# Kernel optimization log

Hardware: AMD Instinct MI355X
Metric: run time of the kernel (lower is better)

## Reference

```python
import jax, jax.numpy as jnp
import numpy as np
from jax import lax

T, B, IN, ND, H, L, C = 128, 64, 48, 3, 2048, 4, 10
MAG = 2.0
U_BOUND = float(np.power(10.0, np.log10(MAG) / T))
INI_IN2HID = 0.02
BN_EPS = 1e-5


def _indrnn_scan(xs, u):
    # xs: [T, B, H], u: [H]; h_t = relu(x_t + u * h_{t-1}), h_0 = 0
    def step(h, xt):
        h = jax.nn.relu(xt + u * h)
        return h, h
    _, hs = lax.scan(step, jnp.zeros_like(xs[0]), xs)
    return hs


def setup_inputs() -> dict:
    key = jax.random.key(0)
    ks = jax.random.split(key, 8)
    x = jax.random.normal(ks[0], (T, B, IN, ND), dtype=jnp.float32)
    W0 = jax.random.uniform(ks[1], (H, IN * ND), minval=-INI_IN2HID, maxval=INI_IN2HID, dtype=jnp.float32)
    Ws = jax.random.uniform(ks[2], (L - 1, H, H), minval=-INI_IN2HID, maxval=INI_IN2HID, dtype=jnp.float32)
    bs = jnp.zeros((L, H), dtype=jnp.float32)
    us = jax.random.uniform(ks[3], (L, H), minval=0.0, maxval=U_BOUND, dtype=jnp.float32)
    gammas = jnp.ones((L, H), dtype=jnp.float32)
    betas = jnp.zeros((L, H), dtype=jnp.float32)
    Wlast = jax.random.normal(ks[4], (C, H), dtype=jnp.float32) * 0.02
    blast = jnp.zeros((C,), dtype=jnp.float32)
    return {"input": x, "W0": W0, "Ws": Ws, "bs": bs, "us": us,
            "gammas": gammas, "betas": betas, "Wlast": Wlast, "blast": blast}


def reference(input, W0, Ws, bs, us, gammas, betas, Wlast, blast):
    t, b, indim, nd = input.shape
    h = input.reshape(t, b, indim * nd)  # [T, B, IN*ND]
    for l in range(L):
        W = W0 if l == 0 else Ws[l - 1]
        # dense input projection (per-timestep Linear)
        z = jnp.einsum('tbi,hi->tbh', h, W) + bs[l]
        # IndRNN only-recurrent: elementwise diagonal recurrence + relu
        h = _indrnn_scan(z, us[l])
        # BatchNorm1d over channel, stats over (time, batch) = training-mode batch stats
        mean = h.mean(axis=(0, 1))
        var = h.var(axis=(0, 1))
        h = (h - mean) * lax.rsqrt(var + BN_EPS) * gammas[l] + betas[l]
        # dropout_overtime skipped (eval mode / training=False -> identity)
    out = h[-1] @ Wlast.T + blast  # last timestep -> [B, C]
    return out
```

## Files before the change

kernel.cpp:

```cpp
#include <hip/hip_runtime.h>

#define T_    128
#define B_    64
#define H_    2048
#define L_    4
#define C_    10
#define BN_EPS 1e-5f
#define K0REAL 144
#define K0PAD  160

typedef __attribute__((ext_vector_type(8))) short bf16x8;
typedef __attribute__((ext_vector_type(4))) float f32x4;

__device__ __forceinline__ short f2bf(float f) {
    union { float f; unsigned u; } v; v.f = f;
    unsigned r = (v.u + 0x7FFFu + ((v.u >> 16) & 1u)) >> 16;
    return (short)r;
}
__device__ __forceinline__ float bf2f(short s) {
    union { unsigned u; float f; } v; v.u = ((unsigned)(unsigned short)s) << 16;
    return v.f;
}
__device__ __forceinline__ void gload16(const short* g, short* l) {
    __builtin_amdgcn_global_load_lds(
        (const __attribute__((address_space(1))) void*)g,
        (__attribute__((address_space(3))) void*)l, 16, 0, 0);
}

#define SBAR() do { __builtin_amdgcn_sched_barrier(0); \
                    __builtin_amdgcn_s_barrier();      \
                    __builtin_amdgcn_sched_barrier(0); } while (0)

__global__ __launch_bounds__(512, 2) void gemm_bf16_8ph(
    const short* __restrict__ A, const short* __restrict__ Bw,
    const float* __restrict__ bias, float* __restrict__ Z,
    int M, int N, int Kb)
{
    __shared__ short As[2][256 * 64];
    __shared__ short Bs[2][256 * 64];

    const int tid  = threadIdx.x;
    const int wid  = tid >> 6;
    const int lane = tid & 63;

    const int lin = blockIdx.y * gridDim.x + blockIdx.x;
    const int m0  = (lin >> 3) * 256;
    const int n0  = (lin & 7) * 256;

    const int wm  = (wid >> 2) * 128;
    const int wn  = (wid & 3) * 64;

    const int fr  = lane & 15;
    const int fq  = lane >> 4;
    const int fr7 = fr & 7;

    const int s_sub   = wid * 2;
    const int s_rowi  = lane >> 3;
    const int s_chunk = (lane & 7) ^ s_rowi;

    auto stA = [&](int kt, int h, int i) {
        const int r = h * 128 + (s_sub + i) * 8 + s_rowi;
        gload16(A + (size_t)(m0 + r) * Kb + kt * 64 + s_chunk * 8,
                &As[kt & 1][h * 8192 + (s_sub + i) * 512 + lane * 8]);
    };
    auto stB = [&](int kt, int h, int i) {
        const int r = h * 128 + (s_sub + i) * 8 + s_rowi;
        gload16(Bw + (size_t)(n0 + r) * Kb + kt * 64 + s_chunk * 8,
                &Bs[kt & 1][h * 8192 + (s_sub + i) * 512 + lane * 8]);
    };
    auto rdA = [&](int buf, int m, int kk) -> bf16x8 {
        const int ar = wm + m * 16 + fr;
        const int slot = (kk * 4 + fq) ^ fr7;
        return *(const bf16x8*)&As[buf][ar * 64 + slot * 8];
    };
    auto rdB = [&](int buf, int n, int kk) -> bf16x8 {
        const int br = wn + n * 16 + fr;
        const int slot = (kk * 4 + fq) ^ fr7;
        return *(const bf16x8*)&Bs[buf][br * 64 + slot * 8];
    };

    f32x4 acc[8][4];
#pragma unroll
    for (int m = 0; m < 8; ++m)
#pragma unroll
        for (int n = 0; n < 4; ++n)
            acc[m][n] = (f32x4){0.f, 0.f, 0.f, 0.f};

    const int NK = Kb >> 6;

    stA(0, 0, 0); stA(0, 0, 1); stA(0, 1, 0); stA(0, 1, 1);
    stB(0, 0, 0); stB(0, 0, 1); stB(0, 1, 0); stB(0, 1, 1);
    stA(1, 0, 0); stA(1, 0, 1); stA(1, 1, 0); stA(1, 1, 1);
    stB(1, 0, 0); stB(1, 0, 1); stB(1, 1, 0); stB(1, 1, 1);
    asm volatile("s_waitcnt vmcnt(8)" ::: "memory");
    SBAR();

    bf16x8 aF[4][2], b0[2][2], b1[2][2];

#pragma unroll 1
    for (int g = 0; g < NK; ++g) {
        const int buf = g & 1;
#pragma unroll
        for (int m = 0; m < 4; ++m)
#pragma unroll
            for (int kk = 0; kk < 2; ++kk) aF[m][kk] = rdA(buf, m, kk);
#pragma unroll
        for (int n = 0; n < 2; ++n)
#pragma unroll
            for (int kk = 0; kk < 2; ++kk) b0[n][kk] = rdB(buf, n, kk);
        SBAR();
        __builtin_amdgcn_s_setprio(1);
#pragma unroll
        for (int m = 0; m < 4; ++m)
#pragma unroll
            for (int n = 0; n < 2; ++n)
#pragma unroll
                for (int kk = 0; kk < 2; ++kk)
                    acc[m][n] = __builtin_amdgcn_mfma_f32_16x16x32_bf16(
                        aF[m][kk], b0[n][kk], acc[m][n], 0, 0, 0);
        __builtin_amdgcn_s_setprio(0);
        SBAR();
#pragma unroll
        for (int n = 0; n < 2; ++n)
#pragma unroll
            for (int kk = 0; kk < 2; ++kk) b1[n][kk] = rdB(buf, n + 2, kk);
        SBAR();
        __builtin_amdgcn_s_setprio(1);
#pragma unroll
        for (int m = 0; m < 4; ++m)
#pragma unroll
            for (int n = 0; n < 2; ++n)
#pragma unroll
                for (int kk = 0; kk < 2; ++kk)
                    acc[m][n + 2] = __builtin_amdgcn_mfma_f32_16x16x32_bf16(
                        aF[m][kk], b1[n][kk], acc[m][n + 2], 0, 0, 0);
        __builtin_amdgcn_s_setprio(0);
        SBAR();
#pragma unroll
        for (int m = 0; m < 4; ++m)
#pragma unroll
            for (int kk = 0; kk < 2; ++kk) aF[m][kk] = rdA(buf, m + 4, kk);
        if (g + 2 < NK) { stB(g + 2, 0, 0); stB(g + 2, 0, 1);
                          stB(g + 2, 1, 0); stB(g + 2, 1, 1); }
        SBAR();
        __builtin_amdgcn_s_setprio(1);
#pragma unroll
        for (int m = 0; m < 4; ++m)
#pragma unroll
            for (int n = 0; n < 2; ++n)
#pragma unroll
                for (int kk = 0; kk < 2; ++kk)
                    acc[m + 4][n + 2] = __builtin_amdgcn_mfma_f32_16x16x32_bf16(
                        aF[m][kk], b1[n][kk], acc[m + 4][n + 2], 0, 0, 0);
        __builtin_amdgcn_s_setprio(0);
        SBAR();
        if (g + 2 < NK) { stA(g + 2, 0, 0); stA(g + 2, 0, 1);
                          stA(g + 2, 1, 0); stA(g + 2, 1, 1); }
        __builtin_amdgcn_s_setprio(1);
#pragma unroll
        for (int m = 0; m < 4; ++m)
#pragma unroll
            for (int n = 0; n < 2; ++n)
#pragma unroll
                for (int kk = 0; kk < 2; ++kk)
                    acc[m + 4][n] = __builtin_amdgcn_mfma_f32_16x16x32_bf16(
                        aF[m][kk], b0[n][kk], acc[m + 4][n], 0, 0, 0);
        __builtin_amdgcn_s_setprio(0);
        if (g + 2 < NK) asm volatile("s_waitcnt vmcnt(8)" ::: "memory");
        else            asm volatile("s_waitcnt vmcnt(0)" ::: "memory");
        SBAR();
    }

#pragma unroll
    for (int m = 0; m < 8; ++m) {
#pragma unroll
        for (int n = 0; n < 4; ++n) {
            const int col = n0 + wn + n * 16 + fr;
            const float bsum = bias[col];
#pragma unroll
            for (int r = 0; r < 4; ++r) {
                const int row = m0 + wm + m * 16 + fq * 4 + r;
                Z[(size_t)row * N + col] = acc[m][n][r] + bsum;
            }
        }
    }
}

__global__ __launch_bounds__(256) void gemm_bf16_lds(
    const short* __restrict__ A, const short* __restrict__ Bw,
    const float* __restrict__ bias,
    float* __restrict__ Z, int M, int N, int Kb)
{
    __shared__ short As[128 * 32];
    __shared__ short Bs[128 * 32];

    const int tid = threadIdx.x;
    const int nwg = gridDim.x * gridDim.y;
    int lin = blockIdx.y * gridDim.x + blockIdx.x;
    lin = (lin & 7) * (nwg >> 3) + (lin >> 3);
    const int bx = lin % gridDim.x;
    const int by = lin / gridDim.x;
    const int m0 = by * 128;
    const int n0 = bx * 128;

    const int srow = tid >> 2;
    const int scol = (tid & 3) * 8;

    const int wid  = tid >> 6;
    const int lane = tid & 63;
    const int wm   = (wid >> 1) * 64;
    const int wn   = (wid & 1) * 64;
    const int fr   = lane & 15;
    const int fk   = (lane >> 4) * 8;

    f32x4 acc[4][4];
#pragma unroll
    for (int m = 0; m < 4; ++m)
#pragma unroll
        for (int n = 0; n < 4; ++n)
            acc[m][n] = (f32x4){0.f, 0.f, 0.f, 0.f};

    const short* Abase = A + (size_t)m0 * Kb;
    const short* Bbase = Bw + (size_t)n0 * Kb;

    for (int k0 = 0; k0 < Kb; k0 += 32) {
        gload16(Abase + (size_t)srow        * Kb + k0 + scol, &As[tid * 8]);
        gload16(Abase + (size_t)(srow + 64) * Kb + k0 + scol, &As[2048 + tid * 8]);
        gload16(Bbase + (size_t)srow        * Kb + k0 + scol, &Bs[tid * 8]);
        gload16(Bbase + (size_t)(srow + 64) * Kb + k0 + scol, &Bs[2048 + tid * 8]);
        __syncthreads();

        bf16x8 af[4], bfv[4];
#pragma unroll
        for (int m = 0; m < 4; ++m)
            af[m] = *(const bf16x8*)&As[(wm + m * 16 + fr) * 32 + fk];
#pragma unroll
        for (int n = 0; n < 4; ++n)
            bfv[n] = *(const bf16x8*)&Bs[(wn + n * 16 + fr) * 32 + fk];

#pragma unroll
        for (int m = 0; m < 4; ++m)
#pragma unroll
            for (int n = 0; n < 4; ++n)
                acc[m][n] = __builtin_amdgcn_mfma_f32_16x16x32_bf16(
                    af[m], bfv[n], acc[m][n], 0, 0, 0);
        __syncthreads();
    }

    const int orow = (lane >> 4) * 4;
#pragma unroll
    for (int m = 0; m < 4; ++m) {
#pragma unroll
        for (int n = 0; n < 4; ++n) {
            const int col = n0 + wn + n * 16 + fr;
            const float bsum = bias[col];
#pragma unroll
            for (int r = 0; r < 4; ++r) {
                const int row = m0 + wm + m * 16 + orow + r;
                Z[(size_t)row * N + col] = acc[m][n][r] + bsum;
            }
        }
    }
}

__global__ __launch_bounds__(256) void scan_bf16(
    const float* __restrict__ Z, const float* __restrict__ u,
    short* __restrict__ Hb, float* __restrict__ sum, float* __restrict__ sumsq)
{
    const int idx = blockIdx.x * blockDim.x + threadIdx.x;
    const int h = idx & (H_ - 1);
    const float uu = u[h];
    float hprev = 0.f, s1 = 0.f, s2 = 0.f;
#pragma unroll 4
    for (int t = 0; t < T_; ++t) {
        const size_t off = (size_t)t * (B_ * H_) + idx;
        float z = Z[off];
        float hv = z + uu * hprev;
        hv = hv > 0.f ? hv : 0.f;
        Hb[off] = f2bf(hv);
        hprev = hv;
        s1 += hv;
        s2 += hv * hv;
    }
    atomicAdd(&sum[h], s1);
    atomicAdd(&sumsq[h], s2);
}

__global__ void bn_finalize(
    const float* __restrict__ sum, const float* __restrict__ sumsq,
    const float* __restrict__ gamma, const float* __restrict__ beta,
    float* __restrict__ scale, float* __restrict__ shift)
{
    const int h = blockIdx.x * blockDim.x + threadIdx.x;
    if (h >= H_) return;
    const float inv_n = 1.f / (float)(T_ * B_);
    const float m = sum[h] * inv_n;
    const float v = sumsq[h] * inv_n - m * m;
    const float s = gamma[h] * rsqrtf(v + BN_EPS);
    scale[h] = s;
    shift[h] = beta[h] - m * s;
}

__global__ __launch_bounds__(256) void fold_wb(
    const float* __restrict__ Wf, const float* __restrict__ scale,
    const float* __restrict__ shift, const float* __restrict__ b,
    short* __restrict__ Wb, float* __restrict__ bias2)
{
    const int wrow = (blockIdx.x * blockDim.x + threadIdx.x) >> 6;
    const int lane = threadIdx.x & 63;
    if (wrow >= H_) return;
    const float* wr = Wf + (size_t)wrow * H_;
    short* wb = Wb + (size_t)wrow * H_;
    float acc = 0.f;
    for (int k4 = lane * 4; k4 < H_; k4 += 256) {
        float4 w  = *(const float4*)(wr + k4);
        float4 sc = *(const float4*)(scale + k4);
        float4 sh = *(const float4*)(shift + k4);
        short4 s;
        s.x = f2bf(w.x * sc.x); s.y = f2bf(w.y * sc.y);
        s.z = f2bf(w.z * sc.z); s.w = f2bf(w.w * sc.w);
        *(short4*)(wb + k4) = s;
        acc += w.x * sh.x + w.y * sh.y + w.z * sh.z + w.w * sh.w;
    }
#pragma unroll
    for (int o = 32; o > 0; o >>= 1) acc += __shfl_down(acc, o);
    if (lane == 0) bias2[wrow] = acc + b[wrow];
}

__global__ __launch_bounds__(256) void conv_pad(
    const float* __restrict__ X, short* __restrict__ Xb, int rows)
{
    const int npr = K0PAD / 4;
    const int idx = blockIdx.x * blockDim.x + threadIdx.x;
    if (idx >= rows * npr) return;
    const int r = idx / npr;
    const int c4 = (idx - r * npr) * 4;
    short4 s = {0, 0, 0, 0};
    if (c4 < K0REAL) {
        float4 v = *(const float4*)(X + (size_t)r * K0REAL + c4);
        s.x = f2bf(v.x); s.y = f2bf(v.y); s.z = f2bf(v.z); s.w = f2bf(v.w);
    }
    *(short4*)(Xb + (size_t)r * K0PAD + c4) = s;
}

__global__ __launch_bounds__(256) void final_proj(
    const short* __restrict__ Hb, const float* __restrict__ scale,
    const float* __restrict__ shift, const float* __restrict__ Wlast,
    const float* __restrict__ blast, float* __restrict__ out)
{
    const int wave = (blockIdx.x * blockDim.x + threadIdx.x) >> 6;
    const int lane = threadIdx.x & 63;
    if (wave >= B_ * C_) return;
    const int b = wave / C_;
    const int c = wave % C_;
    float acc = 0.f;
    for (int h = lane; h < H_; h += 64) {
        float hv = bf2f(Hb[(size_t)b * H_ + h]) * scale[h] + shift[h];
        acc += hv * Wlast[(size_t)c * H_ + h];
    }
#pragma unroll
    for (int o = 32; o > 0; o >>= 1) acc += __shfl_down(acc, o);
    if (lane == 0) out[(size_t)b * C_ + c] = acc + blast[c];
}

extern "C" void kernel_launch(void* const* d_in, const int* in_sizes, int n_in,
                              void* d_out, int out_size, void* d_ws, size_t ws_size,
                              hipStream_t stream)
{
    const float* x      = (const float*)d_in[0];
    const float* W0     = (const float*)d_in[1];
    const float* Ws     = (const float*)d_in[2];
    const float* bs     = (const float*)d_in[3];
    const float* us     = (const float*)d_in[4];
    const float* gammas = (const float*)d_in[5];
    const float* betas  = (const float*)d_in[6];
    const float* Wlast  = (const float*)d_in[7];
    const float* blast  = (const float*)d_in[8];
    float* out = (float*)d_out;

    char* ws = (char*)d_ws;
    float* buf0    = (float*)ws;
    short* Ab      = (short*)(ws + (size_t)64  * 1048576);
    short* Wb      = (short*)(ws + (size_t)96  * 1048576);
    short* X0b     = (short*)(ws + (size_t)104 * 1048576);
    short* W0b     = (short*)(ws + (size_t)107 * 1048576);
    float* sum     = (float*)(ws + (size_t)108 * 1048576);
    float* sumsq   = sum + H_;
    float* bnscale = sumsq + H_;
    float* bnshift = bnscale + H_;
    float* bias2   = bnshift + H_;

    const int M = T_ * B_;

    conv_pad<<<(M * (K0PAD / 4) + 255) / 256, 256, 0, stream>>>(x, X0b, M);
    conv_pad<<<(H_ * (K0PAD / 4) + 255) / 256, 256, 0, stream>>>(W0, W0b, H_);

    gemm_bf16_lds<<<dim3(H_ / 128, M / 128), 256, 0, stream>>>(
        X0b, W0b, bs, buf0, M, H_, K0PAD);

    const dim3 g256(M / 256, H_ / 256);
    for (int l = 0; l < L_; ++l) {
        hipMemsetAsync(sum, 0, 2 * H_ * sizeof(float), stream);
        scan_bf16<<<(B_ * H_) / 256, 256, 0, stream>>>(buf0, us + l * H_, Ab, sum, sumsq);
        bn_finalize<<<H_ / 256, 256, 0, stream>>>(sum, sumsq,
                                                  gammas + l * H_, betas + l * H_,
                                                  bnscale, bnshift);
        if (l < L_ - 1) {
            const float* Wl = Ws + (size_t)l * H_ * H_;
            fold_wb<<<(H_ * 64) / 256, 256, 0, stream>>>(Wl, bnscale, bnshift,
                                                         bs + (l + 1) * H_, Wb, bias2);
            gemm_bf16_8ph<<<g256, 512, 0, stream>>>(Ab, Wb, bias2, buf0, M, H_, H_);
        }
    }

    final_proj<<<(B_ * C_ * 64 + 255) / 256, 256, 0, stream>>>(
        Ab + (size_t)(T_ - 1) * B_ * H_, bnscale, bnshift, Wlast, blast, out);
}
```

Baseline: 445.9 us.

## Store GEMM outputs as bf16, vectorize scan, trim GEMM barriers

```diff
diff --git a/kernel.cpp b/kernel.cpp
--- a/kernel.cpp
+++ b/kernel.cpp
@@ -33,7 +33,7 @@
 
 __global__ __launch_bounds__(512, 2) void gemm_bf16_8ph(
     const short* __restrict__ A, const short* __restrict__ Bw,
-    const float* __restrict__ bias, float* __restrict__ Z,
+    const float* __restrict__ bias, short* __restrict__ Zb,
     int M, int N, int Kb)
 {
     __shared__ short As[2][256 * 64];
@@ -108,7 +108,6 @@
         for (int n = 0; n < 2; ++n)
 #pragma unroll
             for (int kk = 0; kk < 2; ++kk) b0[n][kk] = rdB(buf, n, kk);
-        SBAR();
         __builtin_amdgcn_s_setprio(1);
 #pragma unroll
         for (int m = 0; m < 4; ++m)
@@ -124,7 +123,6 @@
         for (int n = 0; n < 2; ++n)
 #pragma unroll
             for (int kk = 0; kk < 2; ++kk) b1[n][kk] = rdB(buf, n + 2, kk);
-        SBAR();
         __builtin_amdgcn_s_setprio(1);
 #pragma unroll
         for (int m = 0; m < 4; ++m)
@@ -142,7 +140,6 @@
             for (int kk = 0; kk < 2; ++kk) aF[m][kk] = rdA(buf, m + 4, kk);
         if (g + 2 < NK) { stB(g + 2, 0, 0); stB(g + 2, 0, 1);
                           stB(g + 2, 1, 0); stB(g + 2, 1, 1); }
-        SBAR();
         __builtin_amdgcn_s_setprio(1);
 #pragma unroll
         for (int m = 0; m < 4; ++m)
@@ -180,7 +177,7 @@
 #pragma unroll
             for (int r = 0; r < 4; ++r) {
                 const int row = m0 + wm + m * 16 + fq * 4 + r;
-                Z[(size_t)row * N + col] = acc[m][n][r] + bsum;
+                Zb[(size_t)row * N + col] = f2bf(acc[m][n][r] + bsum);
             }
         }
     }
@@ -189,7 +186,7 @@
 __global__ __launch_bounds__(256) void gemm_bf16_lds(
     const short* __restrict__ A, const short* __restrict__ Bw,
     const float* __restrict__ bias,
-    float* __restrict__ Z, int M, int N, int Kb)
+    short* __restrict__ Zb, int M, int N, int Kb)
 {
     __shared__ short As[128 * 32];
     __shared__ short Bs[128 * 32];
@@ -257,33 +254,53 @@
 #pragma unroll
             for (int r = 0; r < 4; ++r) {
                 const int row = m0 + wm + m * 16 + orow + r;
-                Z[(size_t)row * N + col] = acc[m][n][r] + bsum;
+                Zb[(size_t)row * N + col] = f2bf(acc[m][n][r] + bsum);
             }
         }
     }
 }
 
-__global__ __launch_bounds__(256) void scan_bf16(
-    const float* __restrict__ Z, const float* __restrict__ u,
-    short* __restrict__ Hb, float* __restrict__ sum, float* __restrict__ sumsq)
-{
-    const int idx = blockIdx.x * blockDim.x + threadIdx.x;
-    const int h = idx & (H_ - 1);
-    const float uu = u[h];
-    float hprev = 0.f, s1 = 0.f, s2 = 0.f;
-#pragma unroll 4
+__global__ __launch_bounds__(256) void scan_bf16_v2(
+    const short* __restrict__ Zb, const float* __restrict__ u,
+    short* __restrict__ Hb, float* __restrict__ sum, float* __restrict__ sumsq,
+    int store_all)
+{
+    const int tid  = blockIdx.x * blockDim.x + threadIdx.x;
+    const int idx4 = tid * 4;
+    const int h4   = idx4 & (H_ - 1);
+    const float4 uu = *(const float4*)(u + h4);
+    const float uv[4] = {uu.x, uu.y, uu.z, uu.w};
+    float hp[4] = {0.f, 0.f, 0.f, 0.f};
+    float s1[4] = {0.f, 0.f, 0.f, 0.f};
+    float s2[4] = {0.f, 0.f, 0.f, 0.f};
+
+    short4 z0 = *(const short4*)(Zb + idx4);
+    short4 z1 = *(const short4*)(Zb + (size_t)(B_ * H_) + idx4);
+
     for (int t = 0; t < T_; ++t) {
-        const size_t off = (size_t)t * (B_ * H_) + idx;
-        float z = Z[off];
-        float hv = z + uu * hprev;
-        hv = hv > 0.f ? hv : 0.f;
-        Hb[off] = f2bf(hv);
-        hprev = hv;
-        s1 += hv;
-        s2 += hv * hv;
-    }
-    atomicAdd(&sum[h], s1);
-    atomicAdd(&sumsq[h], s2);
+        short4 zc = z0;
+        z0 = z1;
+        if (t + 2 < T_) z1 = *(const short4*)(Zb + (size_t)(t + 2) * (B_ * H_) + idx4);
+        const float zf[4] = {bf2f(zc.x), bf2f(zc.y), bf2f(zc.z), bf2f(zc.w)};
+        short hs[4];
+#pragma unroll
+        for (int j = 0; j < 4; ++j) {
+            float hv = fmaxf(zf[j] + uv[j] * hp[j], 0.f);
+            hp[j] = hv;
+            s1[j] += hv;
+            s2[j] += hv * hv;
+            hs[j] = f2bf(hv);
+        }
+        if (store_all || t == T_ - 1) {
+            short4 o = {hs[0], hs[1], hs[2], hs[3]};
+            *(short4*)(Hb + (size_t)t * (B_ * H_) + idx4) = o;
+        }
+    }
+#pragma unroll
+    for (int j = 0; j < 4; ++j) {
+        atomicAdd(&sum[h4 + j], s1[j]);
+        atomicAdd(&sumsq[h4 + j], s2[j]);
+    }
 }
 
 __global__ void bn_finalize(
@@ -379,12 +396,12 @@
     float* out = (float*)d_out;
 
     char* ws = (char*)d_ws;
-    float* buf0    = (float*)ws;
-    short* Ab      = (short*)(ws + (size_t)64  * 1048576);
-    short* Wb      = (short*)(ws + (size_t)96  * 1048576);
-    short* X0b     = (short*)(ws + (size_t)104 * 1048576);
-    short* W0b     = (short*)(ws + (size_t)107 * 1048576);
-    float* sum     = (float*)(ws + (size_t)108 * 1048576);
+    short* zb      = (short*)ws;
+    short* Ab      = (short*)(ws + (size_t)32 * 1048576);
+    short* Wb      = (short*)(ws + (size_t)64 * 1048576);
+    short* X0b     = (short*)(ws + (size_t)72 * 1048576);
+    short* W0b     = (short*)(ws + (size_t)75 * 1048576);
+    float* sum     = (float*)(ws + (size_t)76 * 1048576);
     float* sumsq   = sum + H_;
     float* bnscale = sumsq + H_;
     float* bnshift = bnscale + H_;
@@ -396,12 +413,13 @@
     conv_pad<<<(H_ * (K0PAD / 4) + 255) / 256, 256, 0, stream>>>(W0, W0b, H_);
 
     gemm_bf16_lds<<<dim3(H_ / 128, M / 128), 256, 0, stream>>>(
-        X0b, W0b, bs, buf0, M, H_, K0PAD);
+        X0b, W0b, bs, zb, M, H_, K0PAD);
 
     const dim3 g256(M / 256, H_ / 256);
     for (int l = 0; l < L_; ++l) {
         hipMemsetAsync(sum, 0, 2 * H_ * sizeof(float), stream);
-        scan_bf16<<<(B_ * H_) / 256, 256, 0, stream>>>(buf0, us + l * H_, Ab, sum, sumsq);
+        scan_bf16_v2<<<(B_ * H_ / 4) / 256, 256, 0, stream>>>(
+            zb, us + l * H_, Ab, sum, sumsq, (l < L_ - 1) ? 1 : 0);
         bn_finalize<<<H_ / 256, 256, 0, stream>>>(sum, sumsq,
                                                   gammas + l * H_, betas + l * H_,
                                                   bnscale, bnshift);
@@ -409,7 +427,7 @@
             const float* Wl = Ws + (size_t)l * H_ * H_;
             fold_wb<<<(H_ * 64) / 256, 256, 0, stream>>>(Wl, bnscale, bnshift,
                                                          bs + (l + 1) * H_, Wb, bias2);
-            gemm_bf16_8ph<<<g256, 512, 0, stream>>>(Ab, Wb, bias2, buf0, M, H_, H_);
+            gemm_bf16_8ph<<<g256, 512, 0, stream>>>(Ab, Wb, bias2, zb, M, H_, H_);
         }
     }
 
```

New measurement: 543.5 us. 1.22x slower.
